# Kernel optimization log

Measured on AMD Instinct MI355X. Metric: run time of the kernel, lower is better.

The kernel has to match this reference:

```python
import jax, jax.numpy as jnp
import numpy as np

NUM_HEADS = 16
HEAD_DIM = 80  # embed_dim 1280 / 16


def setup_inputs() -> dict:
    key = jax.random.key(0)
    ks = jax.random.split(key, 5)
    E = NUM_HEADS * HEAD_DIM
    sq, b = 1024, 8
    x = jax.random.normal(ks[0], (sq, b, E), dtype=jnp.float32)
    w_in = jax.random.normal(ks[1], (E, 3 * E), dtype=jnp.float32) * (E ** -0.5)
    b_in = jax.random.normal(ks[2], (3 * E,), dtype=jnp.float32) * 0.01
    w_out = jax.random.normal(ks[3], (E, E), dtype=jnp.float32) * (E ** -0.5)
    b_out = jax.random.normal(ks[4], (E,), dtype=jnp.float32) * 0.01
    return {"x": x, "w_in": w_in, "b_in": b_in, "w_out": w_out, "b_out": b_out}


def reference(x, w_in, b_in, w_out, b_out):
    sq, b, E = x.shape
    H, D = NUM_HEADS, HEAD_DIM
    norm_factor = jnp.asarray(D ** 0.5, x.dtype)
    # in_proj: [sq, b, 3E] -> [sq, b, H, 3D], split into q/k/v along last dim
    mixed = (x @ w_in + b_in).reshape(sq, b, H, 3 * D)
    q, k, v = jnp.split(mixed, 3, axis=-1)  # each [sq, b, H, D]
    # merge (b, H) and move to batch-of-bmm layout [b*H, sq, D]
    q = q.reshape(sq, b * H, D).transpose(1, 0, 2) / norm_factor
    k = k.reshape(sq, b * H, D).transpose(1, 0, 2)
    v = v.reshape(sq, b * H, D).transpose(1, 0, 2)
    scores = jnp.einsum('nqd,nkd->nqk', q, k)  # [b*H, sq, sq]
    probs = jax.nn.softmax(scores, axis=-1)
    ctx = jnp.einsum('nqk,nkd->nqd', probs, v)  # [b*H, sq, D]
    # [b, H, sq, D] -> [sq, b, H, D] -> [sq, b, E]
    ctx = ctx.reshape(b, H, sq, D).transpose(2, 0, 1, 3).reshape(sq, b, E)
    return ctx @ w_out + b_out
```

## Files before the change

kernel.cpp:

```cpp
#include <hip/hip_runtime.h>

#define DEVI __device__ __forceinline__

typedef _Float16 f16x8 __attribute__((ext_vector_type(8)));
typedef _Float16 f16x4v __attribute__((ext_vector_type(4)));
typedef _Float16 f16x2 __attribute__((ext_vector_type(2)));
typedef __fp16 fp16x2 __attribute__((ext_vector_type(2)));
typedef float f32x4 __attribute__((ext_vector_type(4)));
typedef float f32x16 __attribute__((ext_vector_type(16)));
typedef unsigned u32x4 __attribute__((ext_vector_type(4)));

DEVI void gl16(const void* g, void* l) {
  __builtin_amdgcn_global_load_lds((const __attribute__((address_space(1))) void*)g,
                                   (__attribute__((address_space(3))) void*)l, 16, 0, 0);
}

#define VMCNT(N) asm volatile("s_waitcnt vmcnt(" #N ")" ::: "memory")
#define LGKM0() asm volatile("s_waitcnt lgkmcnt(0)" ::: "memory")
#define BARRIER() asm volatile("s_barrier" ::: "memory")

DEVI unsigned pk2(float a, float b) {
  fp16x2 t = __builtin_amdgcn_cvt_pkrtz(a, b);
  return __builtin_bit_cast(unsigned, t);
}
DEVI void pl32swap(unsigned &a, unsigned &b) {
  asm volatile("v_permlane32_swap_b32 %0, %1" : "+v"(a), "+v"(b));
}

__global__ __launch_bounds__(256) void k_prep(const float* __restrict__ x, _Float16* __restrict__ xb,
                                              const float* __restrict__ w_in, _Float16* __restrict__ w_inT,
                                              const float* __restrict__ w_out, _Float16* __restrict__ w_outT) {
  __shared__ float t[32][33];
  int bid = blockIdx.x;
  int tid = threadIdx.x;
  if (bid < 2048) {
    const int n4 = 8192 * 1280 / 4;
    for (int i = bid * 256 + tid; i < n4; i += 2048 * 256) {
      float4 v = ((const float4*)x)[i];
      f16x4v h = { (_Float16)v.x, (_Float16)v.y, (_Float16)v.z, (_Float16)v.w };
      ((f16x4v*)xb)[i] = h;
    }
    return;
  }
  const float* in; _Float16* out; int R, C, tIdx; bool perm;
  if (bid < 6848) { in = w_in;  out = w_inT;  R = 1280; C = 3840; tIdx = bid - 2048; perm = true; }
  else            { in = w_out; out = w_outT; R = 1280; C = 1280; tIdx = bid - 6848; perm = false; }
  int ntc = C / 32;
  int cb = (tIdx % ntc) * 32, rb = (tIdx / ntc) * 32;
  int tx = tid & 31, ty = tid >> 5;
  #pragma unroll
  for (int i = ty; i < 32; i += 8) t[i][tx] = in[(size_t)(rb + i) * C + cb + tx];
  __syncthreads();
  #pragma unroll
  for (int i = ty; i < 32; i += 8) {
    int c = cb + i;
    if (perm) {
      int hq = c / 240, tt = c - hq * 240;
      int reg = tt / 80, d = tt - reg * 80;
      c = reg * 1280 + hq * 80 + d;
    }
    out[(size_t)c * R + rb + tx] = (_Float16)t[tx][i];
  }
}


#define MM(NLO, AF, BF) do {                                                                       \
    __builtin_amdgcn_s_setprio(1);                                                                 \
    _Pragma("unroll")                                                                              \
    for (int m_ = 0; m_ < 8; m_++) {                                                               \
      acc[m_][NLO]     = __builtin_amdgcn_mfma_f32_16x16x32_f16(AF[m_], BF[NLO],     acc[m_][NLO],     0, 0, 0); \
      acc[m_][NLO + 1] = __builtin_amdgcn_mfma_f32_16x16x32_f16(AF[m_], BF[NLO + 1], acc[m_][NLO + 1], 0, 0, 0); \
    }                                                                                              \
    __builtin_amdgcn_s_setprio(0);                                                                 \
  } while (0)

#define LDA(KT, KK, DST) do {                                                                      \
    const _Float16* bas_ = &smem[(size_t)((((KT) & 1) * 2) + wr) * 8192];                          \
    _Pragma("unroll")                                                                              \
    for (int m_ = 0; m_ < 8; m_++)                                                                 \
      DST[m_] = *(const f16x8*)&bas_[(m_ * 16 + ln) * 64 + (((((KK) * 4) + g) ^ chB) << 3)];       \
  } while (0)

#define LDB(KT, KK, DST) do {                                                                      \
    const _Float16* bas_ = &smem[32768 + (size_t)((((KT) & 1) * 2) + (wc >> 1)) * 8192];           \
    _Pragma("unroll")                                                                              \
    for (int n_ = 0; n_ < 4; n_++)                                                                 \
      DST[n_] = *(const f16x8*)&bas_[((wc & 1) * 64 + n_ * 16 + ln) * 64 + (((((KK) * 4) + g) ^ chB) << 3)]; \
  } while (0)

template<int M, int N, int K>
__global__ __launch_bounds__(512, 2) void k_gemm8(const _Float16* __restrict__ A, const _Float16* __restrict__ BT,
                                                  const float* __restrict__ bias,
                                                  _Float16* __restrict__ qo, _Float16* __restrict__ ko,
                                                  _Float16* __restrict__ vo) {
  extern __shared__ _Float16 smem[];
  constexpr int NT = K / 64;
  constexpr int NI = NT / 2;
  const int tid = threadIdx.x;
  const int w = tid >> 6, lane = tid & 63, ln = lane & 15, g = lane >> 4;
  const int wr = w >> 2, wc = w & 3;
  const int l8 = lane >> 3, l7 = lane & 7;
  const int stChunk = (l7 ^ l8) << 3;
  const int chB = ln & 7;

  constexpr int MT = M / 256;
  const int xcd = blockIdx.x & 7;
  const int i = blockIdx.x >> 3;
  const int bm0 = (xcd * (MT / 8) + (i & 3)) * 256;
  const int bn0 = (i >> 2) * 256;

  auto stgA = [&](int kt, int hh) {
    _Float16* ldsb = &smem[(size_t)((kt & 1) * 2 + hh) * 8192 + w * 1024];
    const _Float16* g0 = &A[(size_t)(bm0 + hh * 128 + w * 16 + l8) * K + kt * 64 + stChunk];
    gl16(g0, ldsb);
    gl16(g0 + (size_t)8 * K, ldsb + 512);
  };
  auto stgB = [&](int kt, int hh) {
    _Float16* ldsb = &smem[32768 + (size_t)((kt & 1) * 2 + hh) * 8192 + w * 1024];
    const _Float16* g0 = &BT[(size_t)(bn0 + hh * 128 + w * 16 + l8) * K + kt * 64 + stChunk];
    gl16(g0, ldsb);
    gl16(g0 + (size_t)8 * K, ldsb + 512);
  };

  f32x4 acc[8][4] = {};
  f16x8 a0[8], a1[8], b0[4], b1[4];

  stgB(0, 0); stgB(0, 1); stgA(0, 0); stgA(0, 1);
  stgB(1, 0); stgB(1, 1); stgA(1, 0);
  VMCNT(6);
  BARRIER();
  LDA(0, 0, a0); LDB(0, 0, b0);

  for (int it = 0; it < NI; ++it) {
    const int T0 = 2 * it, T1 = 2 * it + 1;
    const int S0 = (T0 + 2 < NT) ? T0 + 2 : 0;
    const int S1 = (T1 + 2 < NT) ? T1 + 2 : 1;
    LDB(T0, 1, b1);
    stgA(T1, 1);
    BARRIER();
    MM(0, a0, b0);
    LGKM0(); BARRIER();
    LDA(T0, 1, a1);
    stgB(S0, 0);
    BARRIER();
    MM(2, a0, b0);
    LGKM0(); BARRIER();
    stgB(S0, 1);
    BARRIER();
    MM(0, a1, b1);
    VMCNT(4);
    LGKM0(); BARRIER();
    LDA(T1, 0, a0); LDB(T1, 0, b0);
    stgA(S0, 0);
    BARRIER();
    MM(2, a1, b1);
    LGKM0(); BARRIER();
    LDB(T1, 1, b1);
    stgA(S0, 1);
    BARRIER();
    MM(0, a0, b0);
    LGKM0(); BARRIER();
    LDA(T1, 1, a1);
    stgB(S1, 0);
    BARRIER();
    MM(2, a0, b0);
    LGKM0(); BARRIER();
    stgB(S1, 1);
    BARRIER();
    MM(0, a1, b1);
    VMCNT(4);
    LGKM0(); BARRIER();
    LDA(S0, 0, a0); LDB(S0, 0, b0);
    stgA(S1, 0);
    BARRIER();
    MM(2, a1, b1);
    LGKM0(); BARRIER();
  }

  VMCNT(0);
  BARRIER();
  _Float16* sH = smem;
  const int regn = bn0 / 1280;
  #pragma unroll
  for (int n = 0; n < 4; n++) {
    int col = wc * 64 + n * 16 + ln;
    int rel = bn0 - regn * 1280 + col;
    int h = rel / 80, d = rel - h * 80;
    float bv = bias[h * 240 + regn * 80 + d];
    float scl = (regn == 0) ? (0.11180339887498948f * 1.4426950408889634f) : 1.0f;
    #pragma unroll
    for (int m = 0; m < 8; m++) {
      #pragma unroll
      for (int r = 0; r < 4; r++) {
        int row = wr * 128 + m * 16 + 4 * g + r;
        sH[row * 256 + col] = (_Float16)((acc[m][n][r] + bv) * scl);
      }
    }
  }
  LGKM0();
  BARRIER();
  if (regn < 2) {
    _Float16* dst = regn ? ko : qo;
    #pragma unroll
    for (int i2 = 0; i2 < 16; i2++) {
      int id = tid + 512 * i2;
      int row = id >> 5, c8 = id & 31;
      f16x8 v = *(const f16x8*)&sH[row * 256 + c8 * 8];
      int rel = bn0 - regn * 1280 + c8 * 8;
      int h = rel / 80, d0 = rel - h * 80;
      int grow = bm0 + row;
      *(f16x8*)&dst[(size_t)(((grow & 7) * 16 + h) * 1024 + (grow >> 3)) * 80 + d0] = v;
    }
  } else {
    #pragma unroll
    for (int t = 0; t < 16; t++) {
      int id = tid + 512 * t;
      int col = id & 255, rest = id >> 8;
      int hb = rest & 7, sch = rest >> 3;
      int rel = bn0 - 2560 + col;
      int h = rel / 80, d = rel - h * 80;
      f16x8 v;
      #pragma unroll
      for (int k = 0; k < 8; k++)
        v[k] = sH[(hb + 8 * (sch * 8 + k)) * 256 + col];
      *(f16x8*)&vo[(size_t)((hb * 16 + h) * 80 + d) * 1024 + (bm0 >> 3) + sch * 8] = v;
    }
  }
}

template<int M, int N, int K>
__global__ __launch_bounds__(256) void k_gemm(const _Float16* __restrict__ A, const _Float16* __restrict__ BT,
                                              const float* __restrict__ bias, float* __restrict__ outF) {
  __shared__ _Float16 Al[128 * 32];
  __shared__ _Float16 Bl[128 * 32];
  const int tid = threadIdx.x;
  const int w = tid >> 6, lane = tid & 63, ln = lane & 15, g = lane >> 4;
  const int bm0 = blockIdx.x * 128, bn0 = blockIdx.y * 128;
  const int wm = (w >> 1) * 64, wn = (w & 1) * 64;
  const int r0 = tid >> 2, c0 = (tid & 3) * 8;
  f32x4 acc[4][4] = {};
  for (int kt = 0; kt < K; kt += 32) {
    __syncthreads();
    gl16(&A[(size_t)(bm0 + r0) * K + kt + c0],      &Al[(w * 64) * 8]);
    gl16(&A[(size_t)(bm0 + r0 + 64) * K + kt + c0], &Al[(256 + w * 64) * 8]);
    gl16(&BT[(size_t)(bn0 + r0) * K + kt + c0],      &Bl[(w * 64) * 8]);
    gl16(&BT[(size_t)(bn0 + r0 + 64) * K + kt + c0], &Bl[(256 + w * 64) * 8]);
    __syncthreads();
    f16x8 af[4], bf[4];
    #pragma unroll
    for (int i = 0; i < 4; i++) af[i] = *(const f16x8*)&Al[(wm + i * 16 + ln) * 32 + g * 8];
    #pragma unroll
    for (int i = 0; i < 4; i++) bf[i] = *(const f16x8*)&Bl[(wn + i * 16 + ln) * 32 + g * 8];
    #pragma unroll
    for (int i = 0; i < 4; i++)
      #pragma unroll
      for (int j = 0; j < 4; j++)
        acc[i][j] = __builtin_amdgcn_mfma_f32_16x16x32_f16(af[i], bf[j], acc[i][j], 0, 0, 0);
  }
  #pragma unroll
  for (int j = 0; j < 4; j++) {
    int col = bn0 + wn + j * 16 + ln;
    float bv = bias[col];
    #pragma unroll
    for (int i = 0; i < 4; i++) {
      int mb = bm0 + wm + i * 16 + 4 * g;
      #pragma unroll
      for (int r = 0; r < 4; r++)
        outF[(size_t)(mb + r) * N + col] = acc[i][j][r] + bv;
    }
  }
}

__global__ __launch_bounds__(512, 2) void k_attn(const _Float16* __restrict__ qb, const _Float16* __restrict__ kb,
                                                 const _Float16* __restrict__ vT, _Float16* __restrict__ ctxg) {
  extern __shared__ _Float16 smem[];
  _Float16* Kb0 = smem;
  _Float16* Kb1 = smem + 8192;
  _Float16* Vb0 = smem + 16384;
  _Float16* Vb1 = smem + 16384 + 6144;

  const int tid = threadIdx.x;
  const int w = tid >> 6, lane = tid & 63;
  const int l32 = lane & 31, h = lane >> 5;
  const int lx = l32 & 7;
  const int xcd = blockIdx.x & 7;
  const int j = blockIdx.x >> 3;
  const int head = xcd + 8 * (j & 15);
  const int s0 = (j >> 4) * 256;
  const int bb = head >> 4, h16 = head & 15;

  const int c1 = (tid < 128) ? tid + 512 : tid;
  const int kr0 = tid / 10, kh0 = tid - kr0 * 10;
  const int kr1 = c1 / 10,  kh1 = c1 - kr1 * 10;
  const int vr0 = tid >> 3, vh0 = tid & 7;
  const int vr1 = c1 >> 3,  vh1 = c1 & 7;
  const int kO0 = kr0 * 128 + ((kh0 ^ (kr0 & 7)) << 3);
  const int kO1 = kr1 * 128 + ((kh1 ^ (kr1 & 7)) << 3);
  const int vO0 = vr0 * 64 + ((vh0 ^ (vr0 & 7)) << 3);
  const int vO1 = vr1 * 64 + ((vh1 ^ (vr1 & 7)) << 3);
  const _Float16* kG0 = kb + (size_t)head * 81920 + kr0 * 80 + kh0 * 8;
  const _Float16* kG1 = kb + (size_t)head * 81920 + kr1 * 80 + kh1 * 8;
  const _Float16* vG0 = vT + (size_t)head * 81920 + vr0 * 1024 + vh0 * 8;
  const _Float16* vG1 = vT + (size_t)head * 81920 + vr1 * 1024 + vh1 * 8;

  uint4 krA, krB, vrA, vrB;
  auto issue = [&](int kt) {
    krA = *(const uint4*)(kG0 + kt * 5120);
    krB = *(const uint4*)(kG1 + kt * 5120);
    vrA = *(const uint4*)(vG0 + kt * 64);
    vrB = *(const uint4*)(vG1 + kt * 64);
  };
  auto stage = [&](int b) {
    _Float16* kd = b ? Kb1 : Kb0;
    _Float16* vd = b ? Vb1 : Vb0;
    *(uint4*)(kd + kO0) = krA;
    *(uint4*)(kd + kO1) = krB;
    *(uint4*)(vd + vO0) = vrA;
    *(uint4*)(vd + vO1) = vrB;
  };

  const int qrow = s0 + w * 32 + l32;
  f16x8 qf[5];
  #pragma unroll
  for (int s = 0; s < 5; s++)
    qf[s] = *(const f16x8*)&qb[(size_t)(head * 1024 + qrow) * 80 + s * 16 + h * 8];

  f32x16 ct[3] = {};
  float m_run = -INFINITY, l_run = 0.f;

  issue(0);
  stage(0);
  LGKM0();
  BARRIER();
  issue(1);

  for (int kt = 0; kt < 16; ++kt) {
    const _Float16* kc = (kt & 1) ? Kb1 : Kb0;
    const _Float16* vc = (kt & 1) ? Vb1 : Vb0;

    f32x16 sc0 = {}, sc1 = {};
    __builtin_amdgcn_s_setprio(1);
    #pragma unroll
    for (int s = 0; s < 5; ++s) {
      f16x8 kf0 = *(const f16x8*)&kc[l32 * 128 + (((2 * s + h) ^ lx) << 3)];
      f16x8 kf1 = *(const f16x8*)&kc[(32 + l32) * 128 + (((2 * s + h) ^ lx) << 3)];
      sc0 = __builtin_amdgcn_mfma_f32_32x32x16_f16(kf0, qf[s], sc0, 0, 0, 0);
      sc1 = __builtin_amdgcn_mfma_f32_32x32x16_f16(kf1, qf[s], sc1, 0, 0, 0);
    }
    __builtin_amdgcn_s_setprio(0);

    float mx[8];
    #pragma unroll
    for (int i = 0; i < 8; ++i)
      mx[i] = fmaxf(fmaxf(sc0[i], sc0[i + 8]), fmaxf(sc1[i], sc1[i + 8]));
    #pragma unroll
    for (int i = 0; i < 4; ++i) mx[i] = fmaxf(mx[i], mx[i + 4]);
    float tm = fmaxf(fmaxf(mx[0], mx[2]), fmaxf(mx[1], mx[3]));
    tm = fmaxf(tm, __shfl_xor(tm, 32));

    if (__any(tm > m_run + 8.f)) {
      float mnew = fmaxf(m_run, tm);
      float fac = exp2f(m_run - mnew);
      #pragma unroll
      for (int dt = 0; dt < 3; ++dt)
        #pragma unroll
        for (int i = 0; i < 16; ++i) ct[dt][i] *= fac;
      l_run *= fac;
      m_run = mnew;
    }

    float p0[16], p1[16];
    #pragma unroll
    for (int i = 0; i < 16; ++i) p0[i] = exp2f(sc0[i] - m_run);
    #pragma unroll
    for (int i = 0; i < 16; ++i) p1[i] = exp2f(sc1[i] - m_run);
    float ps = 0.f;
    #pragma unroll
    for (int i = 0; i < 16; ++i) ps += p0[i] + p1[i];

    unsigned fr[4][4];
    #define PACK4(T, PP) do {                                                \
        _Pragma("unroll")                                                    \
        for (int s16 = 0; s16 < 2; ++s16) {                                  \
          unsigned u0 = pk2(PP[8 * s16 + 0], PP[8 * s16 + 1]);               \
          unsigned u1 = pk2(PP[8 * s16 + 2], PP[8 * s16 + 3]);               \
          unsigned u2 = pk2(PP[8 * s16 + 4], PP[8 * s16 + 5]);               \
          unsigned u3 = pk2(PP[8 * s16 + 6], PP[8 * s16 + 7]);               \
          pl32swap(u0, u2); pl32swap(u1, u3);                                \
          fr[2 * (T) + s16][0] = u0; fr[2 * (T) + s16][1] = u1;              \
          fr[2 * (T) + s16][2] = u2; fr[2 * (T) + s16][3] = u3;              \
        }                                                                    \
      } while (0)
    PACK4(0, p0);
    PACK4(1, p1);

    l_run += ps + __shfl_xor(ps, 32);

    __builtin_amdgcn_s_setprio(1);
    #pragma unroll
    for (int ss = 0; ss < 4; ++ss) {
      u32x4 fu = { fr[ss][0], fr[ss][1], fr[ss][2], fr[ss][3] };
      f16x8 pf = __builtin_bit_cast(f16x8, fu);
      #pragma unroll
      for (int dt = 0; dt < 3; ++dt) {
        f16x8 vf = *(const f16x8*)&vc[(dt * 32 + l32) * 64 + (((2 * ss + h) ^ lx) << 3)];
        ct[dt] = __builtin_amdgcn_mfma_f32_32x32x16_f16(vf, pf, ct[dt], 0, 0, 0);
      }
    }
    __builtin_amdgcn_s_setprio(0);

    if (kt < 15) {
      stage((kt + 1) & 1);
      LGKM0();
      BARRIER();
      if (kt < 14) issue(kt + 2);
    }
  }

  float inv = 1.f / l_run;
  int sq = s0 + w * 32 + l32;
  _Float16* outp = ctxg + (size_t)(sq * 8 + bb) * 1280 + h16 * 80 + 4 * h;
  #pragma unroll
  for (int dt = 0; dt < 3; ++dt)
    #pragma unroll
    for (int rq = 0; rq < 4; ++rq) {
      if (dt == 2 && rq >= 2) continue;
      f16x4v o = { (_Float16)(ct[dt][rq * 4 + 0] * inv), (_Float16)(ct[dt][rq * 4 + 1] * inv),
                   (_Float16)(ct[dt][rq * 4 + 2] * inv), (_Float16)(ct[dt][rq * 4 + 3] * inv) };
      *(f16x4v*)&outp[dt * 32 + rq * 8] = o;
    }
}

extern "C" void kernel_launch(void* const* d_in, const int* in_sizes, int n_in,
                              void* d_out, int out_size, void* d_ws, size_t ws_size,
                              hipStream_t stream) {
  const float* x     = (const float*)d_in[0];
  const float* w_in  = (const float*)d_in[1];
  const float* b_in  = (const float*)d_in[2];
  const float* w_out = (const float*)d_in[3];
  const float* b_out = (const float*)d_in[4];
  float* out = (float*)d_out;

  char* ws = (char*)d_ws;
  size_t off = 0;
  auto carve = [&](size_t bytes) -> void* {
    void* p = ws + off;
    off += (bytes + 255) & ~(size_t)255;
    return p;
  };
  _Float16* xb     = (_Float16*)carve(8192ull * 1280 * 2);
  _Float16* w_inT  = (_Float16*)carve(3840ull * 1280 * 2);
  _Float16* w_outT = (_Float16*)carve(1280ull * 1280 * 2);
  _Float16* qb     = (_Float16*)carve(128ull * 1024 * 80 * 2);
  _Float16* kbuf   = (_Float16*)carve(128ull * 1024 * 80 * 2);
  _Float16* vT     = (_Float16*)carve(128ull * 1024 * 80 * 2);
  _Float16* ctxg   = (_Float16*)carve(8192ull * 1280 * 2);
  if (off > ws_size) return;

  hipFuncSetAttribute(reinterpret_cast<const void*>(&k_gemm8<8192, 3840, 1280>),
                      hipFuncAttributeMaxDynamicSharedMemorySize, 131072);
  hipFuncSetAttribute(reinterpret_cast<const void*>(&k_attn),
                      hipFuncAttributeMaxDynamicSharedMemorySize, 57344);

  k_prep<<<8448, 256, 0, stream>>>(x, xb, w_in, w_inT, w_out, w_outT);

  k_gemm8<8192, 3840, 1280><<<480, 512, 131072, stream>>>(xb, w_inT, b_in, qb, kbuf, vT);
  k_attn<<<512, 512, 57344, stream>>>(qb, kbuf, vT, ctxg);
  k_gemm<8192, 1280, 1280><<<dim3(64, 10), 256, 0, stream>>>(ctxg, w_outT, b_out, out);
}
```

Before: 240.1 us.

## Pipeline output projection GEMM and move V transpose from QKV epilogue into attention

Replaces the simple single-buffered 128x128 output-projection GEMM with a 512-thread, 128x256-tile kernel. The new kernel double-buffers swizzled LDS tiles loaded with global_load_lds, interleaves MFMAs with fragment loads under setprio, and maps blocks with XCD awareness. The QKV GEMM epilogue now writes V in the same row layout as Q and K, dropping the strided transposing gather. The attention kernel instead transposes V with scalar LDS stores while staging. Main aim is better MFMA utilisation in the final GEMM. The V change trades epilogue cost for more LDS store instructions inside the attention loop.

```diff
diff --git a/kernel.cpp b/kernel.cpp
--- a/kernel.cpp
+++ b/kernel.cpp
@@ -181,10 +181,11 @@
   BARRIER();
   _Float16* sH = smem;
   const int regn = bn0 / 1280;
+  const int relb = bn0 - regn * 1280;
   #pragma unroll
   for (int n = 0; n < 4; n++) {
     int col = wc * 64 + n * 16 + ln;
-    int rel = bn0 - regn * 1280 + col;
+    int rel = relb + col;
     int h = rel / 80, d = rel - h * 80;
     float bv = bias[h * 240 + regn * 80 + d];
     float scl = (regn == 0) ? (0.11180339887498948f * 1.4426950408889634f) : 1.0f;
@@ -199,80 +200,127 @@
   }
   LGKM0();
   BARRIER();
-  if (regn < 2) {
-    _Float16* dst = regn ? ko : qo;
-    #pragma unroll
-    for (int i2 = 0; i2 < 16; i2++) {
-      int id = tid + 512 * i2;
-      int row = id >> 5, c8 = id & 31;
-      f16x8 v = *(const f16x8*)&sH[row * 256 + c8 * 8];
-      int rel = bn0 - regn * 1280 + c8 * 8;
-      int h = rel / 80, d0 = rel - h * 80;
-      int grow = bm0 + row;
-      *(f16x8*)&dst[(size_t)(((grow & 7) * 16 + h) * 1024 + (grow >> 3)) * 80 + d0] = v;
-    }
-  } else {
-    #pragma unroll
-    for (int t = 0; t < 16; t++) {
-      int id = tid + 512 * t;
-      int col = id & 255, rest = id >> 8;
-      int hb = rest & 7, sch = rest >> 3;
-      int rel = bn0 - 2560 + col;
-      int h = rel / 80, d = rel - h * 80;
-      f16x8 v;
-      #pragma unroll
-      for (int k = 0; k < 8; k++)
-        v[k] = sH[(hb + 8 * (sch * 8 + k)) * 256 + col];
-      *(f16x8*)&vo[(size_t)((hb * 16 + h) * 80 + d) * 1024 + (bm0 >> 3) + sch * 8] = v;
-    }
-  }
-}
+  _Float16* dst = (regn == 0) ? qo : (regn == 1) ? ko : vo;
+  #pragma unroll
+  for (int i2 = 0; i2 < 16; i2++) {
+    int id = tid + 512 * i2;
+    int row = id >> 5, c8 = id & 31;
+    f16x8 v = *(const f16x8*)&sH[row * 256 + c8 * 8];
+    int rel = relb + c8 * 8;
+    int h = rel / 80, d0 = rel - h * 80;
+    int grow = bm0 + row;
+    *(f16x8*)&dst[(size_t)(((grow & 7) * 16 + h) * 1024 + (grow >> 3)) * 80 + d0] = v;
+  }
+}
+
+
+#define MMo(NLO, AF, BF) do {                                                                      \
+    __builtin_amdgcn_s_setprio(1);                                                                 \
+    _Pragma("unroll")                                                                              \
+    for (int m_ = 0; m_ < 4; m_++) {                                                               \
+      acc[m_][NLO]     = __builtin_amdgcn_mfma_f32_16x16x32_f16(AF[m_], BF[NLO],     acc[m_][NLO],     0, 0, 0); \
+      acc[m_][NLO + 1] = __builtin_amdgcn_mfma_f32_16x16x32_f16(AF[m_], BF[NLO + 1], acc[m_][NLO + 1], 0, 0, 0); \
+    }                                                                                              \
+    __builtin_amdgcn_s_setprio(0);                                                                 \
+  } while (0)
+
+#define LDAo(KT, KK, DST) do {                                                                     \
+    const _Float16* bas_ = &smem[(size_t)((KT) & 1) * 8192];                                       \
+    _Pragma("unroll")                                                                              \
+    for (int m_ = 0; m_ < 4; m_++)                                                                 \
+      DST[m_] = *(const f16x8*)&bas_[(wr * 64 + m_ * 16 + ln) * 64 + (((((KK) * 4) + g) ^ chB) << 3)]; \
+  } while (0)
+
+#define LDBo(KT, KK, DST) do {                                                                     \
+    const _Float16* bas_ = &smem[16384 + (size_t)(((KT) & 1) * 2 + (wc >> 1)) * 8192];             \
+    _Pragma("unroll")                                                                              \
+    for (int n_ = 0; n_ < 4; n_++)                                                                 \
+      DST[n_] = *(const f16x8*)&bas_[((wc & 1) * 64 + n_ * 16 + ln) * 64 + (((((KK) * 4) + g) ^ chB) << 3)]; \
+  } while (0)
 
 template<int M, int N, int K>
-__global__ __launch_bounds__(256) void k_gemm(const _Float16* __restrict__ A, const _Float16* __restrict__ BT,
-                                              const float* __restrict__ bias, float* __restrict__ outF) {
-  __shared__ _Float16 Al[128 * 32];
-  __shared__ _Float16 Bl[128 * 32];
+__global__ __launch_bounds__(512, 2) void k_gemm8o(const _Float16* __restrict__ A, const _Float16* __restrict__ BT,
+                                                   const float* __restrict__ bias, float* __restrict__ outF) {
+  extern __shared__ _Float16 smem[];
+  constexpr int NT = K / 64;
+  constexpr int NI = NT / 2;
   const int tid = threadIdx.x;
   const int w = tid >> 6, lane = tid & 63, ln = lane & 15, g = lane >> 4;
-  const int bm0 = blockIdx.x * 128, bn0 = blockIdx.y * 128;
-  const int wm = (w >> 1) * 64, wn = (w & 1) * 64;
-  const int r0 = tid >> 2, c0 = (tid & 3) * 8;
+  const int wr = w >> 2, wc = w & 3;
+  const int l8 = lane >> 3, l7 = lane & 7;
+  const int stChunk = (l7 ^ l8) << 3;
+  const int chB = ln & 7;
+
+  const int xcd = blockIdx.x & 7;
+  const int i = blockIdx.x >> 3;
+  const int bm0 = (xcd * 8 + (i & 7)) * 128;
+  const int bn0 = (i >> 3) * 256;
+
+  auto stgA = [&](int kt) {
+    _Float16* ldsb = &smem[(size_t)(kt & 1) * 8192 + w * 1024];
+    const _Float16* g0 = &A[(size_t)(bm0 + w * 16 + l8) * K + kt * 64 + stChunk];
+    gl16(g0, ldsb);
+    gl16(g0 + (size_t)8 * K, ldsb + 512);
+  };
+  auto stgB = [&](int kt, int hh) {
+    _Float16* ldsb = &smem[16384 + (size_t)((kt & 1) * 2 + hh) * 8192 + w * 1024];
+    const _Float16* g0 = &BT[(size_t)(bn0 + hh * 128 + w * 16 + l8) * K + kt * 64 + stChunk];
+    gl16(g0, ldsb);
+    gl16(g0 + (size_t)8 * K, ldsb + 512);
+  };
+
   f32x4 acc[4][4] = {};
-  for (int kt = 0; kt < K; kt += 32) {
-    __syncthreads();
-    gl16(&A[(size_t)(bm0 + r0) * K + kt + c0],      &Al[(w * 64) * 8]);
-    gl16(&A[(size_t)(bm0 + r0 + 64) * K + kt + c0], &Al[(256 + w * 64) * 8]);
-    gl16(&BT[(size_t)(bn0 + r0) * K + kt + c0],      &Bl[(w * 64) * 8]);
-    gl16(&BT[(size_t)(bn0 + r0 + 64) * K + kt + c0], &Bl[(256 + w * 64) * 8]);
-    __syncthreads();
-    f16x8 af[4], bf[4];
-    #pragma unroll
-    for (int i = 0; i < 4; i++) af[i] = *(const f16x8*)&Al[(wm + i * 16 + ln) * 32 + g * 8];
-    #pragma unroll
-    for (int i = 0; i < 4; i++) bf[i] = *(const f16x8*)&Bl[(wn + i * 16 + ln) * 32 + g * 8];
-    #pragma unroll
-    for (int i = 0; i < 4; i++)
-      #pragma unroll
-      for (int j = 0; j < 4; j++)
-        acc[i][j] = __builtin_amdgcn_mfma_f32_16x16x32_f16(af[i], bf[j], acc[i][j], 0, 0, 0);
-  }
-  #pragma unroll
-  for (int j = 0; j < 4; j++) {
-    int col = bn0 + wn + j * 16 + ln;
+  f16x8 a0[4], a1[4], b0[4], b1[4];
+
+  stgB(0, 0); stgB(0, 1); stgA(0);
+  stgB(1, 0); stgB(1, 1); stgA(1);
+  VMCNT(6);
+  BARRIER();
+  LDAo(0, 0, a0); LDBo(0, 0, b0);
+
+  for (int it = 0; it < NI; ++it) {
+    const int T0 = 2 * it, T1 = 2 * it + 1;
+    const int S0 = (T0 + 2 < NT) ? T0 + 2 : 0;
+    const int S1 = (T1 + 2 < NT) ? T1 + 2 : 1;
+    LDBo(T0, 1, b1);
+    BARRIER(); MMo(0, a0, b0); LGKM0(); BARRIER();
+    LDAo(T0, 1, a1);
+    stgB(S0, 0);
+    BARRIER(); MMo(2, a0, b0); LGKM0(); BARRIER();
+    stgB(S0, 1);
+    BARRIER(); MMo(0, a1, b1); VMCNT(4); LGKM0(); BARRIER();
+    LDAo(T1, 0, a0); LDBo(T1, 0, b0);
+    stgA(S0);
+    BARRIER(); MMo(2, a1, b1); LGKM0(); BARRIER();
+    LDBo(T1, 1, b1);
+    BARRIER(); MMo(0, a0, b0); LGKM0(); BARRIER();
+    LDAo(T1, 1, a1);
+    stgB(S1, 0);
+    BARRIER(); MMo(2, a0, b0); LGKM0(); BARRIER();
+    stgB(S1, 1);
+    BARRIER(); MMo(0, a1, b1); VMCNT(4); LGKM0(); BARRIER();
+    LDAo(S0, 0, a0); LDBo(S0, 0, b0);
+    stgA(S1);
+    BARRIER(); MMo(2, a1, b1); LGKM0(); BARRIER();
+  }
+
+  VMCNT(0);
+  #pragma unroll
+  for (int n = 0; n < 4; n++) {
+    int col = bn0 + wc * 64 + n * 16 + ln;
     float bv = bias[col];
     #pragma unroll
-    for (int i = 0; i < 4; i++) {
-      int mb = bm0 + wm + i * 16 + 4 * g;
+    for (int m = 0; m < 4; m++) {
+      int rbase = bm0 + wr * 64 + m * 16 + 4 * g;
       #pragma unroll
       for (int r = 0; r < 4; r++)
-        outF[(size_t)(mb + r) * N + col] = acc[i][j][r] + bv;
+        outF[(size_t)(rbase + r) * N + col] = acc[m][n][r] + bv;
     }
   }
 }
 
 __global__ __launch_bounds__(512, 2) void k_attn(const _Float16* __restrict__ qb, const _Float16* __restrict__ kb,
-                                                 const _Float16* __restrict__ vT, _Float16* __restrict__ ctxg) {
+                                                 const _Float16* __restrict__ vb, _Float16* __restrict__ ctxg) {
   extern __shared__ _Float16 smem[];
   _Float16* Kb0 = smem;
   _Float16* Kb1 = smem + 8192;
@@ -289,34 +337,39 @@
   const int s0 = (j >> 4) * 256;
   const int bb = head >> 4, h16 = head & 15;
 
-  const int c1 = (tid < 128) ? tid + 512 : tid;
-  const int kr0 = tid / 10, kh0 = tid - kr0 * 10;
-  const int kr1 = c1 / 10,  kh1 = c1 - kr1 * 10;
-  const int vr0 = tid >> 3, vh0 = tid & 7;
-  const int vr1 = c1 >> 3,  vh1 = c1 & 7;
-  const int kO0 = kr0 * 128 + ((kh0 ^ (kr0 & 7)) << 3);
-  const int kO1 = kr1 * 128 + ((kh1 ^ (kr1 & 7)) << 3);
-  const int vO0 = vr0 * 64 + ((vh0 ^ (vr0 & 7)) << 3);
-  const int vO1 = vr1 * 64 + ((vh1 ^ (vr1 & 7)) << 3);
-  const _Float16* kG0 = kb + (size_t)head * 81920 + kr0 * 80 + kh0 * 8;
-  const _Float16* kG1 = kb + (size_t)head * 81920 + kr1 * 80 + kh1 * 8;
-  const _Float16* vG0 = vT + (size_t)head * 81920 + vr0 * 1024 + vh0 * 8;
-  const _Float16* vG1 = vT + (size_t)head * 81920 + vr1 * 1024 + vh1 * 8;
+  const int cA = tid;
+  const int cB = (tid < 128) ? tid + 512 : tid;
+  const int sA = cA & 63, dA = cA >> 6;
+  const int sB = cB & 63, dB = cB >> 6;
+  const size_t hbase = (size_t)head * 81920;
+  const _Float16* kGA = kb + hbase + sA * 80 + dA * 8;
+  const _Float16* kGB = kb + hbase + sB * 80 + dB * 8;
+  const _Float16* vGA = vb + hbase + sA * 80 + dA * 8;
+  const _Float16* vGB = vb + hbase + sB * 80 + dB * 8;
+  const int kOA = sA * 128 + ((dA ^ (sA & 7)) << 3);
+  const int kOB = sB * 128 + ((dB ^ (sB & 7)) << 3);
 
   uint4 krA, krB, vrA, vrB;
   auto issue = [&](int kt) {
-    krA = *(const uint4*)(kG0 + kt * 5120);
-    krB = *(const uint4*)(kG1 + kt * 5120);
-    vrA = *(const uint4*)(vG0 + kt * 64);
-    vrB = *(const uint4*)(vG1 + kt * 64);
+    krA = *(const uint4*)(kGA + kt * 5120);
+    krB = *(const uint4*)(kGB + kt * 5120);
+    vrA = *(const uint4*)(vGA + kt * 5120);
+    vrB = *(const uint4*)(vGB + kt * 5120);
   };
   auto stage = [&](int b) {
     _Float16* kd = b ? Kb1 : Kb0;
     _Float16* vd = b ? Vb1 : Vb0;
-    *(uint4*)(kd + kO0) = krA;
-    *(uint4*)(kd + kO1) = krB;
-    *(uint4*)(vd + vO0) = vrA;
-    *(uint4*)(vd + vO1) = vrB;
+    *(uint4*)(kd + kOA) = krA;
+    *(uint4*)(kd + kOB) = krB;
+    f16x8 va = __builtin_bit_cast(f16x8, vrA);
+    f16x8 vbv = __builtin_bit_cast(f16x8, vrB);
+    #pragma unroll
+    for (int jj = 0; jj < 8; ++jj) {
+      int da = dA * 8 + jj;
+      vd[da * 64 + (((sA >> 3) ^ (da & 7)) << 3) + (sA & 7)] = va[jj];
+      int db = dB * 8 + jj;
+      vd[db * 64 + (((sB >> 3) ^ (db & 7)) << 3) + (sB & 7)] = vbv[jj];
+    }
   };
 
   const int qrow = s0 + w * 32 + l32;
@@ -453,18 +506,20 @@
   _Float16* w_outT = (_Float16*)carve(1280ull * 1280 * 2);
   _Float16* qb     = (_Float16*)carve(128ull * 1024 * 80 * 2);
   _Float16* kbuf   = (_Float16*)carve(128ull * 1024 * 80 * 2);
-  _Float16* vT     = (_Float16*)carve(128ull * 1024 * 80 * 2);
+  _Float16* vbuf   = (_Float16*)carve(128ull * 1024 * 80 * 2);
   _Float16* ctxg   = (_Float16*)carve(8192ull * 1280 * 2);
   if (off > ws_size) return;
 
   hipFuncSetAttribute(reinterpret_cast<const void*>(&k_gemm8<8192, 3840, 1280>),
                       hipFuncAttributeMaxDynamicSharedMemorySize, 131072);
+  hipFuncSetAttribute(reinterpret_cast<const void*>(&k_gemm8o<8192, 1280, 1280>),
+                      hipFuncAttributeMaxDynamicSharedMemorySize, 98304);
   hipFuncSetAttribute(reinterpret_cast<const void*>(&k_attn),
                       hipFuncAttributeMaxDynamicSharedMemorySize, 57344);
 
   k_prep<<<8448, 256, 0, stream>>>(x, xb, w_in, w_inT, w_out, w_outT);
 
-  k_gemm8<8192, 3840, 1280><<<480, 512, 131072, stream>>>(xb, w_inT, b_in, qb, kbuf, vT);
-  k_attn<<<512, 512, 57344, stream>>>(qb, kbuf, vT, ctxg);
-  k_gemm<8192, 1280, 1280><<<dim3(64, 10), 256, 0, stream>>>(ctxg, w_outT, b_out, out);
-}
+  k_gemm8<8192, 3840, 1280><<<480, 512, 131072, stream>>>(xb, w_inT, b_in, qb, kbuf, vbuf);
+  k_attn<<<512, 512, 57344, stream>>>(qb, kbuf, vbuf, ctxg);
+  k_gemm8o<8192, 1280, 1280><<<320, 512, 98304, stream>>>(ctxg, w_outT, b_out, out);
+}
```

Result: slower. 245.5 us (+2.3%).
